# Kernel tuning notes

Measured on AMD Instinct MI355X. Metric: run time of the kernel, lower is better.

## Reference

```python
import jax, jax.numpy as jnp
import numpy as np

H = 16; W = 16; C_IN = 32; RNN_IN = 64; HID = 128; OUT = 512; B = 512


def _upsample_bilinear_ac(x, oh, ow):
    """Bilinear upsample with align_corners=True (matches nn.UpsamplingBilinear2d). x: (B,C,h,w)."""
    h, w = x.shape[2], x.shape[3]
    ys = (jnp.arange(oh, dtype=jnp.float32) * (h - 1) / (oh - 1))
    y0 = jnp.floor(ys).astype(jnp.int32)
    y1 = jnp.minimum(y0 + 1, h - 1)
    wy = (ys - y0.astype(jnp.float32))[None, None, :, None]
    xs = (jnp.arange(ow, dtype=jnp.float32) * (w - 1) / (ow - 1))
    x0 = jnp.floor(xs).astype(jnp.int32)
    x1 = jnp.minimum(x0 + 1, w - 1)
    wx = (xs - x0.astype(jnp.float32))[None, None, None, :]
    rows = x[:, :, y0, :] * (1.0 - wy) + x[:, :, y1, :] * wy  # (B,C,oh,w)
    out = rows[:, :, :, x0] * (1.0 - wx) + rows[:, :, :, x1] * wx  # (B,C,oh,ow)
    return out


def setup_inputs() -> dict:
    key = jax.random.key(0)
    ks = jax.random.split(key, 8)
    def winit(k, shape, fan_in):
        return jax.random.normal(k, shape, jnp.float32) / np.float32(np.sqrt(fan_in))
    return {
        "x": jax.random.normal(ks[0], (B, C_IN, H, W), jnp.float32),
        "h0": jax.random.normal(ks[1], (B, HID), jnp.float32),
        "W_in": winit(ks[2], (RNN_IN, C_IN), C_IN),
        "b_in": jnp.zeros((RNN_IN,), jnp.float32),
        "W_ih": winit(ks[3], (HID, RNN_IN), RNN_IN),
        "b_ih": jnp.zeros((HID,), jnp.float32),
        "W_hh": winit(ks[4], (HID, HID), HID),
        "b_hh": jnp.zeros((HID,), jnp.float32),
        "W_out": winit(ks[5], (OUT, HID), HID),
        "b_out": jnp.zeros((OUT,), jnp.float32),
    }


def reference(x, h0, W_in, b_in, W_ih, b_ih, W_hh, b_hh, W_out, b_out):
    b = x.shape[0]
    # (B,C,H,W) -> (B,L,C), L = H*W raster order
    x_seq = x.transpose(0, 2, 3, 1).reshape(b, H * W, C_IN)
    proj = x_seq @ W_in.T + b_in                      # (B,L,RNN_IN)
    pre = proj @ W_ih.T + b_ih                        # (B,L,HID), input part of RNNCell precomputed

    def step(h, p_t):
        h_new = jnp.tanh(p_t + h @ W_hh.T + b_hh)
        return h_new, h_new

    _, hs = jax.lax.scan(step, h0, pre.transpose(1, 0, 2))  # (L,B,HID)
    hs_map = hs.reshape(H, W, b, HID).transpose(2, 3, 0, 1)  # (B,HID,H,W)
    up = _upsample_bilinear_ac(hs_map, 2 * H, 2 * W)         # (B,HID,32,32)
    act = up * jnp.clip(up + 3.0, 0.0, 6.0) * (1.0 / 6.0)    # hardswish
    pooled = act.mean(axis=(2, 3))                           # (B,HID)
    return pooled @ W_out.T + b_out
```

## Files before the change

### kernel.cpp

```cpp
#include <hip/hip_runtime.h>

#define L 256
#define BATCH 512
#define CIN 32
#define HIDN 128
#define OUTN 512

typedef _Float16 f16x8 __attribute__((ext_vector_type(8)));
typedef float f32x4 __attribute__((ext_vector_type(4)));

#define MFMA16(a, b, c) __builtin_amdgcn_mfma_f32_16x16x32_f16(a, b, c, 0, 0, 0)

static __device__ __forceinline__ unsigned short f16b(_Float16 h) {
    unsigned short u; __builtin_memcpy(&u, &h, 2); return u;
}


__global__ __launch_bounds__(256) void prep_kernel(
    const float* __restrict__ W_in, const float* __restrict__ b_in,
    const float* __restrict__ W_ih, const float* __restrict__ b_ih,
    const float* __restrict__ b_hh, const float* __restrict__ Whh,
    unsigned short* __restrict__ Wh, unsigned short* __restrict__ Wl,
    unsigned short* __restrict__ Wch, unsigned short* __restrict__ Wcl,
    float* __restrict__ bpre)
{
    const int tid = threadIdx.x;
    __shared__ float win[64 * CIN];
    for (int i = tid; i < 64 * CIN; i += 256) win[i] = W_in[i];
    __syncthreads();
    if (tid < 128) {
        const int j = tid;
        float acc[CIN];
#pragma unroll
        for (int c = 0; c < CIN; ++c) acc[c] = 0.f;
        float bs = b_ih[j] + b_hh[j];
        for (int m = 0; m < 64; ++m) {
            float w = W_ih[j * 64 + m];
            bs += w * b_in[m];
#pragma unroll
            for (int c = 0; c < CIN; ++c) acc[c] += w * win[m * CIN + c];
        }
        bpre[j] = bs;
#pragma unroll
        for (int c = 0; c < CIN; ++c) {
            _Float16 h = (_Float16)acc[c];
            _Float16 l = (_Float16)(acc[c] - (float)h);
            Wch[j * CIN + c] = f16b(h);
            Wcl[j * CIN + c] = f16b(l);
        }
    } else {
        const int j = tid - 128;
        for (int k = 0; k < HIDN; k += 4) {
            float4 v = *(const float4*)(Whh + j * HIDN + k);
            float vv[4] = {v.x, v.y, v.z, v.w};
#pragma unroll
            for (int u = 0; u < 4; ++u) {
                _Float16 h = (_Float16)vv[u];
                _Float16 l = (_Float16)(vv[u] - (float)h);
                Wh[j * HIDN + k + u] = f16b(h);
                Wl[j * HIDN + k + u] = f16b(l);
            }
        }
    }
}

__global__ __launch_bounds__(512, 1) void rnn_kernel(
    const float* __restrict__ x, const float* __restrict__ h0,
    const unsigned short* __restrict__ Wh, const unsigned short* __restrict__ Wl,
    const unsigned short* __restrict__ Wch, const unsigned short* __restrict__ Wcl,
    const float* __restrict__ bpre, unsigned short* __restrict__ hs)
{
    const int tid = threadIdx.x;
    const int bb = blockIdx.x;
    const int lane = tid & 63;
    const int w = tid >> 6;
    const int n = lane & 15;
    const int q = lane >> 4;

    __shared__ unsigned short hbuf[2][16][HIDN];
    __shared__ unsigned short xc[2][16][16][CIN];

    f16x8 Ah[4], Al[4], Axh, Axl;
    const int jr = w * 16 + n;
#pragma unroll
    for (int kc = 0; kc < 4; ++kc) {
        Ah[kc] = *(const f16x8*)(Wh + jr * HIDN + kc * 32 + q * 8);
        Al[kc] = *(const f16x8*)(Wl + jr * HIDN + kc * 32 + q * 8);
    }
    Axh = *(const f16x8*)(Wch + jr * CIN + q * 8);
    Axl = *(const f16x8*)(Wcl + jr * CIN + q * 8);
    float4 bv = *(const float4*)(bpre + w * 16 + q * 4);
    f32x4 bp = (f32x4){bv.x, bv.y, bv.z, bv.w};

    if (tid < 256) {
        const int ni = tid >> 4, gi = tid & 15;
        const float4* src = (const float4*)(h0 + ((size_t)bb * 16 + ni) * HIDN + gi * 8);
        float4 a = src[0], b4 = src[1];
        float vv[8] = {a.x, a.y, a.z, a.w, b4.x, b4.y, b4.z, b4.w};
        unsigned short o[8];
#pragma unroll
        for (int i = 0; i < 8; ++i) o[i] = f16b((_Float16)vv[i]);
        *(uint4*)&hbuf[0][ni][(gi ^ (ni & 7)) * 8] = *(uint4*)o;
    }

    float4 xr[4];
    auto issue_chunk = [&](int ci) {
#pragma unroll
        for (int r = 0; r < 4; ++r) {
            int i = tid + r * 512;
            int nn = i >> 7, cc = (i >> 2) & 31, tq = i & 3;
            xr[r] = *(const float4*)(x + (((size_t)bb * 16 + nn) * CIN + cc) * L + ci * 16 + tq * 4);
        }
    };
    auto write_chunk = [&](int buf) {
#pragma unroll
        for (int r = 0; r < 4; ++r) {
            int i = tid + r * 512;
            int nn = i >> 7, cc = (i >> 2) & 31, tq = i & 3;
            float vv[4] = {xr[r].x, xr[r].y, xr[r].z, xr[r].w};
#pragma unroll
            for (int k = 0; k < 4; ++k)
                xc[buf][tq * 4 + k][nn][cc] = f16b((_Float16)vv[k]);
        }
    };

    issue_chunk(0);
    write_chunk(0);
    issue_chunk(1);
    __syncthreads();

    unsigned short* hsp = hs + ((size_t)bb * 16 + n) * HIDN + w * 16 + q * 4;

    for (int t = 0; t < L; ++t) {
        const int p = t & 1;
        const int cb = (t >> 4) & 1, tt = t & 15;

        f16x8 Bh[4];
#pragma unroll
        for (int kc = 0; kc < 4; ++kc)
            Bh[kc] = *(const f16x8*)&hbuf[p][n][((4 * kc + q) ^ (n & 7)) * 8];
        f16x8 xB = *(const f16x8*)&xc[cb][tt][n][q * 8];

        f32x4 aH = bp;
        f32x4 aL = (f32x4){0.f, 0.f, 0.f, 0.f};
#pragma unroll
        for (int kc = 0; kc < 4; ++kc) {
            aH = MFMA16(Ah[kc], Bh[kc], aH);
            aL = MFMA16(Al[kc], Bh[kc], aL);
        }
        aH = MFMA16(Axh, xB, aH);
        aL = MFMA16(Axl, xB, aL);

        if (tt == 15 && t < L - 16) {
            write_chunk(cb ^ 1);
            if (t < L - 32) issue_chunk((t >> 4) + 2);
        }

        f32x4 acc = aH + aL;
        unsigned short o[4];
#pragma unroll
        for (int r = 0; r < 4; ++r) {
            float e = __expf(2.f * acc[r]);
            float hv = 1.f - 2.f * __builtin_amdgcn_rcpf(e + 1.f);
            o[r] = f16b((_Float16)hv);
        }
        uint2 pk; __builtin_memcpy(&pk, o, 8);
        const int G = (w * 2 + (q >> 1)) ^ (n & 7);
        *(uint2*)&hbuf[p ^ 1][n][G * 8 + (q & 1) * 4] = pk;
        *(uint2*)(hsp + (size_t)t * (BATCH * HIDN)) = pk;

        asm volatile("" ::: "memory");
        __builtin_amdgcn_s_waitcnt(0xC07F);
        __builtin_amdgcn_s_barrier();
        asm volatile("" ::: "memory");
    }
}

__global__ __launch_bounds__(256) void pool_out_kernel(
    const unsigned short* __restrict__ hs, const float* __restrict__ W_out,
    const float* __restrict__ b_out, float* __restrict__ out)
{
    const int b = blockIdx.x, tid = threadIdx.x;
    __shared__ unsigned short m[L][HIDN];
    __shared__ float ps[2][HIDN];
    __shared__ float pooled_s[HIDN];

#pragma unroll
    for (int it = 0; it < 16; ++it) {
        int i = tid + it * 256;
        int t = i >> 4, g = i & 15;
        *(uint4*)&m[t][g * 8] =
            *(const uint4*)(hs + (size_t)t * (BATCH * HIDN) + b * HIDN + g * 8);
    }
    __syncthreads();

    const int jo = tid & 127, sub = tid >> 7;
    float acc = 0.f;
    for (int oy = sub * 16; oy < sub * 16 + 16; ++oy) {
        float ysf = oy * (15.f / 31.f);
        int y0 = (int)ysf; float wy = ysf - (float)y0; int y1 = min(y0 + 1, 15);
        float rb[16];
#pragma unroll
        for (int sx = 0; sx < 16; ++sx) {
            float v0 = (float)*(const _Float16*)&m[y0 * 16 + sx][jo];
            float v1 = (float)*(const _Float16*)&m[y1 * 16 + sx][jo];
            rb[sx] = v0 + wy * (v1 - v0);
        }
#pragma unroll
        for (int ox = 0; ox < 32; ++ox) {
            float xsf = ox * (15.f / 31.f);
            int x0 = (int)xsf; float wx = xsf - (float)x0; int x1 = min(x0 + 1, 15);
            float v = rb[x0] + wx * (rb[x1] - rb[x0]);
            float t6 = fminf(fmaxf(v + 3.f, 0.f), 6.f);
            acc += v * t6;
        }
    }
    ps[sub][jo] = acc;
    __syncthreads();
    if (tid < 128) pooled_s[tid] = (ps[0][tid] + ps[1][tid]) * (1.f / 6144.f);
    __syncthreads();

    for (int o = tid; o < OUTN; o += 256) {
        float a = b_out[o];
#pragma unroll 8
        for (int k = 0; k < HIDN; k += 4) {
            float4 wv = *(const float4*)(W_out + o * HIDN + k);
            float4 pv = *(const float4*)&pooled_s[k];
            a += wv.x * pv.x + wv.y * pv.y + wv.z * pv.z + wv.w * pv.w;
        }
        out[b * OUTN + o] = a;
    }
}

extern "C" void kernel_launch(void* const* d_in, const int* in_sizes, int n_in,
                              void* d_out, int out_size, void* d_ws, size_t ws_size,
                              hipStream_t stream)
{
    const float* x     = (const float*)d_in[0];
    const float* h0    = (const float*)d_in[1];
    const float* W_in  = (const float*)d_in[2];
    const float* b_in  = (const float*)d_in[3];
    const float* W_ih  = (const float*)d_in[4];
    const float* b_ih  = (const float*)d_in[5];
    const float* W_hh  = (const float*)d_in[6];
    const float* b_hh  = (const float*)d_in[7];
    const float* W_out = (const float*)d_in[8];
    const float* b_out = (const float*)d_in[9];
    float* out = (float*)d_out;

    char* wsb = (char*)d_ws;
    unsigned short* Wh  = (unsigned short*)(wsb);
    unsigned short* Wl  = (unsigned short*)(wsb + 32768);
    unsigned short* Wch = (unsigned short*)(wsb + 65536);
    unsigned short* Wcl = (unsigned short*)(wsb + 73728);
    float* bpre         = (float*)(wsb + 81920);
    unsigned short* hsb = (unsigned short*)(wsb + 98304);

    prep_kernel<<<1, 256, 0, stream>>>(W_in, b_in, W_ih, b_ih, b_hh, W_hh,
                                       Wh, Wl, Wch, Wcl, bpre);
    rnn_kernel<<<32, 512, 0, stream>>>(x, h0, Wh, Wl, Wch, Wcl, bpre, hsb);
    pool_out_kernel<<<512, 256, 0, stream>>>(hsb, W_out, b_out, out);
}
```

Before: 227.1 us.

## Unroll RNN steps per chunk, split MFMA chains, batch hs stores

Result: slower. 264.0 us (+16.3%).

```diff
diff --git a/kernel.cpp b/kernel.cpp
--- a/kernel.cpp
+++ b/kernel.cpp
@@ -80,6 +80,8 @@
     __shared__ unsigned short hbuf[2][16][HIDN];
     __shared__ unsigned short xc[2][16][16][CIN];
 
+    const f32x4 ZERO4 = {0.f, 0.f, 0.f, 0.f};
+
     f16x8 Ah[4], Al[4], Axh, Axl;
     const int jr = w * 16 + n;
 #pragma unroll
@@ -90,7 +92,7 @@
     Axh = *(const f16x8*)(Wch + jr * CIN + q * 8);
     Axl = *(const f16x8*)(Wcl + jr * CIN + q * 8);
     float4 bv = *(const float4*)(bpre + w * 16 + q * 4);
-    f32x4 bp = (f32x4){bv.x, bv.y, bv.z, bv.w};
+    f32x4 bp = {bv.x, bv.y, bv.z, bv.w};
 
     if (tid < 256) {
         const int ni = tid >> 4, gi = tid & 15;
@@ -131,48 +133,60 @@
 
     unsigned short* hsp = hs + ((size_t)bb * 16 + n) * HIDN + w * 16 + q * 4;
 
-    for (int t = 0; t < L; ++t) {
-        const int p = t & 1;
-        const int cb = (t >> 4) & 1, tt = t & 15;
-
-        f16x8 Bh[4];
-#pragma unroll
-        for (int kc = 0; kc < 4; ++kc)
-            Bh[kc] = *(const f16x8*)&hbuf[p][n][((4 * kc + q) ^ (n & 7)) * 8];
-        f16x8 xB = *(const f16x8*)&xc[cb][tt][n][q * 8];
-
-        f32x4 aH = bp;
-        f32x4 aL = (f32x4){0.f, 0.f, 0.f, 0.f};
-#pragma unroll
-        for (int kc = 0; kc < 4; ++kc) {
-            aH = MFMA16(Ah[kc], Bh[kc], aH);
-            aL = MFMA16(Al[kc], Bh[kc], aL);
-        }
-        aH = MFMA16(Axh, xB, aH);
-        aL = MFMA16(Axl, xB, aL);
-
-        if (tt == 15 && t < L - 16) {
-            write_chunk(cb ^ 1);
-            if (t < L - 32) issue_chunk((t >> 4) + 2);
-        }
-
-        f32x4 acc = aH + aL;
-        unsigned short o[4];
-#pragma unroll
-        for (int r = 0; r < 4; ++r) {
-            float e = __expf(2.f * acc[r]);
-            float hv = 1.f - 2.f * __builtin_amdgcn_rcpf(e + 1.f);
-            o[r] = f16b((_Float16)hv);
-        }
-        uint2 pk; __builtin_memcpy(&pk, o, 8);
-        const int G = (w * 2 + (q >> 1)) ^ (n & 7);
-        *(uint2*)&hbuf[p ^ 1][n][G * 8 + (q & 1) * 4] = pk;
-        *(uint2*)(hsp + (size_t)t * (BATCH * HIDN)) = pk;
-
-        asm volatile("" ::: "memory");
-        __builtin_amdgcn_s_waitcnt(0xC07F);
-        __builtin_amdgcn_s_barrier();
-        asm volatile("" ::: "memory");
+    f16x8 xB, xBn;
+    uint2 hsbuf[16];
+
+    for (int c16 = 0; c16 < 16; ++c16) {
+        const int cb = c16 & 1;
+#pragma unroll
+        for (int tt = 0; tt < 16; ++tt) {
+            const int p = tt & 1;
+
+            f16x8 Bh[4];
+#pragma unroll
+            for (int kc = 0; kc < 4; ++kc)
+                Bh[kc] = *(const f16x8*)&hbuf[p][n][((4 * kc + q) ^ (n & 7)) * 8];
+            if (tt == 0) xB = *(const f16x8*)&xc[cb][0][n][q * 8];
+            if (tt < 15) xBn = *(const f16x8*)&xc[cb][tt + 1][n][q * 8];
+
+            f32x4 c1 = MFMA16(Axh, xB, ZERO4);
+            f32x4 c2 = MFMA16(Axl, xB, ZERO4);
+            c1 = MFMA16(Ah[0], Bh[0], c1);
+            c2 = MFMA16(Al[0], Bh[0], c2);
+            f32x4 c0 = MFMA16(Ah[1], Bh[1], bp);
+            f32x4 c3 = MFMA16(Al[1], Bh[1], ZERO4);
+            c1 = MFMA16(Ah[2], Bh[2], c1);
+            c2 = MFMA16(Al[2], Bh[2], c2);
+            c0 = MFMA16(Ah[3], Bh[3], c0);
+            c3 = MFMA16(Al[3], Bh[3], c3);
+            f32x4 acc = (c0 + c1) + (c2 + c3);
+
+            unsigned short o[4];
+#pragma unroll
+            for (int r = 0; r < 4; ++r) {
+                float e = __expf(2.f * acc[r]);
+                float hv = 1.f - 2.f * __builtin_amdgcn_rcpf(e + 1.f);
+                o[r] = f16b((_Float16)hv);
+            }
+            uint2 pk; __builtin_memcpy(&pk, o, 8);
+            const int G = (w * 2 + (q >> 1)) ^ (n & 7);
+            *(uint2*)&hbuf[p ^ 1][n][G * 8 + (q & 1) * 4] = pk;
+            hsbuf[tt] = pk;
+
+            if (tt == 15) {
+#pragma unroll
+                for (int k = 0; k < 16; ++k)
+                    *(uint2*)(hsp + (size_t)(c16 * 16 + k) * (BATCH * HIDN)) = hsbuf[k];
+                if (c16 < 15) write_chunk(cb ^ 1);
+                if (c16 < 14) issue_chunk(c16 + 2);
+            }
+
+            asm volatile("" ::: "memory");
+            __builtin_amdgcn_s_waitcnt(0xC07F);
+            __builtin_amdgcn_s_barrier();
+            asm volatile("" ::: "memory");
+            xB = xBn;
+        }
     }
 }
 
```
